# Optimization experiments

Hardware: AMD Instinct MI355X
Metric: run time of the kernel (lower is better)

The kernel has to match this reference:

```python
import jax, jax.numpy as jnp
import numpy as np

N_NODES = 50000
N_EDGES = 800000
IN_CH = 128
OUT_CH = 64
SELF_LOOP_W = 2.0  # improved=True in GCNConv


def setup_inputs() -> dict:
    key = jax.random.key(0)
    k1, k2, k3, k4 = jax.random.split(key, 4)
    x = jax.random.normal(k1, (N_NODES, IN_CH), dtype=jnp.float32)
    edge_index = jax.random.randint(k2, (2, N_EDGES), 0, N_NODES, dtype=jnp.int64)
    edge_weight = jax.random.uniform(k3, (N_EDGES,), dtype=jnp.float32)
    W = jax.random.normal(k4, (IN_CH, OUT_CH), dtype=jnp.float32) / np.sqrt(IN_CH)
    b = jnp.zeros((OUT_CH,), dtype=jnp.float32)
    return {"x": x, "edge_index": edge_index, "edge_weight": edge_weight, "W": W, "b": b}


def reference(x, edge_index, edge_weight, W, b):
    # Only the first GCNConv layer runs (the torch loop returns after k=0).
    N = x.shape[0]
    row, col = edge_index[0], edge_index[1]  # source, target

    # gcn_norm with add_self_loops=True, improved=True (fill value 2.0)
    loop_idx = jnp.arange(N, dtype=edge_index.dtype)
    row_f = jnp.concatenate([row, loop_idx])
    col_f = jnp.concatenate([col, loop_idx])
    ew_f = jnp.concatenate([edge_weight, jnp.full((N,), SELF_LOOP_W, dtype=edge_weight.dtype)])

    deg = jax.ops.segment_sum(ew_f, col_f, num_segments=N)          # [N]
    dinv = jnp.where(deg > 0, jax.lax.rsqrt(deg), 0.0)
    norm = dinv[row_f] * ew_f * dinv[col_f]                          # [E+N]

    # linear transform then normalized sparse aggregation
    xw = x @ W                                                       # [N, out]
    msg = norm[:, None] * xw[row_f]                                  # [E+N, out] gather
    out = jax.ops.segment_sum(msg, col_f, num_segments=N)           # [N, out] scatter-add
    return out + b
```

## Files before the change

kernel.cpp:

```cpp
#include <hip/hip_runtime.h>

constexpr int N    = 50000;
constexpr int E    = 800000;
constexpr int CIN  = 128;
constexpr int COUT = 64;
constexpr float SELF_LOOP_W = 2.0f;

constexpr int NB   = (N + 63) / 64;
constexpr int CAP  = 1536;
constexpr int EPB  = 2048;
constexpr int PBLK = (E + EPB - 1) / EPB;

typedef float          vfloat4  __attribute__((ext_vector_type(4)));
typedef int            vint2    __attribute__((ext_vector_type(2)));
typedef int            vint4    __attribute__((ext_vector_type(4)));
typedef unsigned short vushort4 __attribute__((ext_vector_type(4)));

__device__ __forceinline__ unsigned short f2bf(float f) {
    unsigned int u = __float_as_uint(f);
    u += 0x7FFFu + ((u >> 16) & 1u);
    return (unsigned short)(u >> 16);
}
__device__ __forceinline__ float bf2f(unsigned short h) {
    return __uint_as_float(((unsigned int)h) << 16);
}

__global__ __launch_bounds__(512) void partition_kernel(const int* __restrict__ row,
                                                        const int* __restrict__ col,
                                                        const float* __restrict__ ew,
                                                        int* __restrict__ bcur,
                                                        vint2* __restrict__ pk) {
    __shared__ int lhist[NB];
    __shared__ int lbase[NB];
    const int t  = threadIdx.x;
    const int e  = blockIdx.x * EPB + t * 4;
    const bool valid = (e < E);

    for (int i = t; i < NB; i += 512) lhist[i] = 0;
    __syncthreads();

    vint4 c4;
    if (valid) {
        c4 = *(const vint4*)(col + e);
        #pragma unroll
        for (int u = 0; u < 4; ++u) atomicAdd(&lhist[c4[u] >> 6], 1);
    }
    __syncthreads();

    for (int i = t; i < NB; i += 512) {
        int h = lhist[i];
        if (h > 0) lbase[i] = i * CAP + atomicAdd(&bcur[i], h);
    }
    __syncthreads();

    if (valid) {
        vint4   r4 = *(const vint4*)(row + e);
        vfloat4 w4 = *(const vfloat4*)(ew + e);
        #pragma unroll
        for (int u = 0; u < 4; ++u) {
            int c   = c4[u];
            int bkt = c >> 6;
            int p   = atomicAdd(&lbase[bkt], 1);
            if (p < (bkt + 1) * CAP) {
                vint2 v;
                v.x = r4[u] | ((c & 63) << 20);
                v.y = __float_as_int(w4[u]);
                pk[p] = v;
            }
        }
    }
}

__global__ __launch_bounds__(256) void xw_deg_kernel(const float* __restrict__ x,
                                                     const float* __restrict__ W,
                                                     const int* __restrict__ bcur,
                                                     const vint2* __restrict__ pk,
                                                     unsigned short* __restrict__ xwh,
                                                     float* __restrict__ dinv) {
    __shared__ __align__(16) float xs[64][132];
    __shared__ float ldeg[64];

    const int t    = threadIdx.x;
    const int b    = blockIdx.x;
    const int base = b * 64;

    #pragma unroll
    for (int i = 0; i < 8; ++i) {
        int f4  = i * 256 + t;
        int r   = f4 >> 5;
        int c4  = f4 & 31;
        int node = base + r;
        if (node >= N) node = N - 1;
        vfloat4 v = *(const vfloat4*)(x + (size_t)node * CIN + c4 * 4);
        *(vfloat4*)&xs[r][c4 * 4] = v;
    }
    if (t < 64) ldeg[t] = 0.f;
    __syncthreads();

    const int tc = t & 15;
    const int tn = t >> 4;

    float acc[4][4];
    #pragma unroll
    for (int i = 0; i < 4; ++i)
        #pragma unroll
        for (int j = 0; j < 4; ++j) acc[i][j] = 0.f;

    const float* Wp = W + tc * 4;
    #pragma unroll 8
    for (int k = 0; k < CIN; ++k) {
        vfloat4 bv = *(const vfloat4*)(Wp + (size_t)k * COUT);
        float a0 = xs[tn * 4 + 0][k];
        float a1 = xs[tn * 4 + 1][k];
        float a2 = xs[tn * 4 + 2][k];
        float a3 = xs[tn * 4 + 3][k];
        #pragma unroll
        for (int j = 0; j < 4; ++j) {
            acc[0][j] += a0 * bv[j];
            acc[1][j] += a1 * bv[j];
            acc[2][j] += a2 * bv[j];
            acc[3][j] += a3 * bv[j];
        }
    }

    #pragma unroll
    for (int i = 0; i < 4; ++i) {
        int node = base + tn * 4 + i;
        if (node >= N) continue;
        vushort4 hv;
        #pragma unroll
        for (int j = 0; j < 4; ++j) hv[j] = f2bf(acc[i][j]);
        *(vushort4*)(xwh + (size_t)node * COUT + tc * 4) = hv;
    }

    const int pbase = b * CAP;
    const int cnt   = min(bcur[b], CAP);
    for (int j = t; j < cnt; j += 256) {
        vint2 v = pk[pbase + j];
        atomicAdd(&ldeg[(v.x >> 20) & 63], __int_as_float(v.y));
    }
    __syncthreads();
    int node = base + t;
    if (t < 64 && node < N) dinv[node] = rsqrtf(SELF_LOOP_W + ldeg[t]);
}

__global__ __launch_bounds__(512) void aggregate_kernel(const int* __restrict__ bcur,
                                                        const vint2* __restrict__ pk,
                                                        const float* __restrict__ dinv,
                                                        const unsigned short* __restrict__ xwh,
                                                        const float* __restrict__ bias,
                                                        float* __restrict__ out) {
    __shared__ int   rawx[CAP];
    __shared__ float rawn[CAP];
    __shared__ int   s_r[CAP];
    __shared__ float s_n[CAP];
    __shared__ int   lhist[64], lofs[64], lcur[64];

    const int t    = threadIdx.x;
    const int lane = t & 63;
    const int wv   = t >> 6;
    const int b    = blockIdx.x;
    const int base = b * CAP;
    const int cnt  = min(bcur[b], CAP);

    if (t < 64) lhist[t] = 0;
    __syncthreads();

    for (int j = t; j < cnt; j += 512) {
        vint2 v = pk[base + j];
        rawx[j] = v.x;
        rawn[j] = __int_as_float(v.y) * dinv[v.x & 0xFFFFF];
        atomicAdd(&lhist[(v.x >> 20) & 63], 1);
    }
    __syncthreads();

    if (t < 64) {
        int v = lhist[t];
        int s = v;
        #pragma unroll
        for (int d = 1; d < 64; d <<= 1) {
            int u = __shfl_up(s, d);
            if (lane >= d) s += u;
        }
        lofs[t] = s - v;
        lcur[t] = s - v;
    }
    __syncthreads();

    for (int j = t; j < cnt; j += 512) {
        int xv = rawx[j];
        int p  = atomicAdd(&lcur[(xv >> 20) & 63], 1);
        s_r[p] = xv & 0xFFFFF;
        s_n[p] = rawn[j];
    }
    __syncthreads();

    const int q  = lane >> 4;
    const int c4 = lane & 15;

    for (int nd = wv; nd < 64; nd += 8) {
        int node = b * 64 + nd;
        if (node >= N) continue;
        int s0 = lofs[nd];
        int e0 = s0 + lhist[nd];

        float a0 = 0.f, a1 = 0.f, a2 = 0.f, a3 = 0.f;
        for (int i = s0; i < e0; i += 16) {
            int rr[4]; float nn[4]; vushort4 vv[4];
            #pragma unroll
            for (int u = 0; u < 4; ++u) {
                int j = i + 4 * u + q;
                bool ok = (j < e0);
                rr[u] = ok ? s_r[j] : s_r[s0];
                nn[u] = ok ? s_n[j] : 0.f;
            }
            #pragma unroll
            for (int u = 0; u < 4; ++u)
                vv[u] = *(const vushort4*)(xwh + (size_t)rr[u] * COUT + c4 * 4);
            #pragma unroll
            for (int u = 0; u < 4; ++u) {
                a0 += nn[u] * bf2f(vv[u][0]);
                a1 += nn[u] * bf2f(vv[u][1]);
                a2 += nn[u] * bf2f(vv[u][2]);
                a3 += nn[u] * bf2f(vv[u][3]);
            }
        }
        a0 += __shfl_xor(a0, 16); a0 += __shfl_xor(a0, 32);
        a1 += __shfl_xor(a1, 16); a1 += __shfl_xor(a1, 32);
        a2 += __shfl_xor(a2, 16); a2 += __shfl_xor(a2, 32);
        a3 += __shfl_xor(a3, 16); a3 += __shfl_xor(a3, 32);

        if (q == 0) {
            float dc = dinv[node];
            float s2 = SELF_LOOP_W * dc * dc;
            vushort4 sh = *(const vushort4*)(xwh + (size_t)node * COUT + c4 * 4);
            vfloat4  bv = *(const vfloat4*)(bias + c4 * 4);
            vfloat4  o;
            o[0] = dc * a0 + s2 * bf2f(sh[0]) + bv[0];
            o[1] = dc * a1 + s2 * bf2f(sh[1]) + bv[1];
            o[2] = dc * a2 + s2 * bf2f(sh[2]) + bv[2];
            o[3] = dc * a3 + s2 * bf2f(sh[3]) + bv[3];
            *(vfloat4*)(out + (size_t)node * COUT + c4 * 4) = o;
        }
    }
}

extern "C" void kernel_launch(void* const* d_in, const int* in_sizes, int n_in,
                              void* d_out, int out_size, void* d_ws, size_t ws_size,
                              hipStream_t stream) {
    const float* x  = (const float*)d_in[0];
    const int*   ei = (const int*)d_in[1];
    const float* ew = (const float*)d_in[2];
    const float* W  = (const float*)d_in[3];
    const float* b  = (const float*)d_in[4];
    float* out = (float*)d_out;

    unsigned short* xwh  = (unsigned short*)d_ws;
    float*          dinv = (float*)(xwh + (size_t)N * COUT);
    int*            bcur = (int*)(dinv + N);
    vint2*          pk   = (vint2*)(bcur + NB + 2);

    const int* rowp = ei;
    const int* colp = ei + E;

    hipMemsetAsync(bcur, 0, NB * sizeof(int), stream);
    partition_kernel<<<PBLK, 512, 0, stream>>>(rowp, colp, ew, bcur, pk);
    xw_deg_kernel   <<<NB, 256, 0, stream>>>(x, W, bcur, pk, xwh, dinv);
    aggregate_kernel<<<NB, 512, 0, stream>>>(bcur, pk, dinv, xwh, b, out);
}
```

Baseline: 149.9 us.

## Fuse edge partitioning with XW transform and compute degrees via global atomics

Merges the partition kernel and the xw/degree kernel into one launch with NB blocks, each handling 64 nodes of the XW product and 1024 edges of partitioning. Degree is now accumulated with global float atomics during partitioning, and rsqrt is computed on the fly in the aggregate kernel instead of storing dinv. This removes a launch and a second pass over the packed edge buffer, but adds 800K global atomics and repeated rsqrt/deg gathers in aggregation.

```diff
diff --git a/kernel.cpp b/kernel.cpp
--- a/kernel.cpp
+++ b/kernel.cpp
@@ -8,12 +8,10 @@
 
 constexpr int NB   = (N + 63) / 64;
 constexpr int CAP  = 1536;
-constexpr int EPB  = 2048;
-constexpr int PBLK = (E + EPB - 1) / EPB;
 
 typedef float          vfloat4  __attribute__((ext_vector_type(4)));
+typedef float          vfloat2  __attribute__((ext_vector_type(2)));
 typedef int            vint2    __attribute__((ext_vector_type(2)));
-typedef int            vint4    __attribute__((ext_vector_type(4)));
 typedef unsigned short vushort4 __attribute__((ext_vector_type(4)));
 
 __device__ __forceinline__ unsigned short f2bf(float f) {
@@ -25,25 +23,48 @@
     return __uint_as_float(((unsigned int)h) << 16);
 }
 
-__global__ __launch_bounds__(512) void partition_kernel(const int* __restrict__ row,
-                                                        const int* __restrict__ col,
-                                                        const float* __restrict__ ew,
-                                                        int* __restrict__ bcur,
-                                                        vint2* __restrict__ pk) {
+__global__ __launch_bounds__(512) void partition_xw_kernel(
+        const int* __restrict__ row, const int* __restrict__ col,
+        const float* __restrict__ ew, const float* __restrict__ x,
+        const float* __restrict__ W,
+        int* __restrict__ bcur, float* __restrict__ deg,
+        vint2* __restrict__ pk, unsigned short* __restrict__ xwh) {
     __shared__ int lhist[NB];
     __shared__ int lbase[NB];
-    const int t  = threadIdx.x;
-    const int e  = blockIdx.x * EPB + t * 4;
-    const bool valid = (e < E);
-
+    __shared__ __align__(16) float xs[64][132];
+
+    const int t    = threadIdx.x;
+    const int b    = blockIdx.x;
+    const int base = b * 64;
+
+    #pragma unroll
+    for (int i = 0; i < 4; ++i) {
+        int f4 = i * 512 + t;
+        int r  = f4 >> 5;
+        int c4 = f4 & 31;
+        int node = base + r;
+        if (node >= N) node = N - 1;
+        *(vfloat4*)&xs[r][c4 * 4] = *(const vfloat4*)(x + (size_t)node * CIN + c4 * 4);
+    }
     for (int i = t; i < NB; i += 512) lhist[i] = 0;
-    __syncthreads();
-
-    vint4 c4;
+
+    const int e0 = b * 1024 + t * 2;
+    const bool valid = (e0 < E);
+    vint2 c2 = {0, 0}, r2 = {0, 0};
+    vfloat2 w2 = {0.f, 0.f};
     if (valid) {
-        c4 = *(const vint4*)(col + e);
-        #pragma unroll
-        for (int u = 0; u < 4; ++u) atomicAdd(&lhist[c4[u] >> 6], 1);
+        c2 = *(const vint2*)(col + e0);
+        r2 = *(const vint2*)(row + e0);
+        w2 = *(const vfloat2*)(ew + e0);
+    }
+    __syncthreads();
+
+    if (valid) {
+        #pragma unroll
+        for (int u = 0; u < 2; ++u) {
+            atomicAdd(&lhist[c2[u] >> 6], 1);
+            atomicAdd(&deg[c2[u]], w2[u]);
+        }
     }
     __syncthreads();
 
@@ -54,55 +75,25 @@
     __syncthreads();
 
     if (valid) {
-        vint4   r4 = *(const vint4*)(row + e);
-        vfloat4 w4 = *(const vfloat4*)(ew + e);
-        #pragma unroll
-        for (int u = 0; u < 4; ++u) {
-            int c   = c4[u];
+        #pragma unroll
+        for (int u = 0; u < 2; ++u) {
+            int c   = c2[u];
             int bkt = c >> 6;
             int p   = atomicAdd(&lbase[bkt], 1);
             if (p < (bkt + 1) * CAP) {
                 vint2 v;
-                v.x = r4[u] | ((c & 63) << 20);
-                v.y = __float_as_int(w4[u]);
+                v.x = r2[u] | ((c & 63) << 20);
+                v.y = __float_as_int(w2[u]);
                 pk[p] = v;
             }
         }
     }
-}
-
-__global__ __launch_bounds__(256) void xw_deg_kernel(const float* __restrict__ x,
-                                                     const float* __restrict__ W,
-                                                     const int* __restrict__ bcur,
-                                                     const vint2* __restrict__ pk,
-                                                     unsigned short* __restrict__ xwh,
-                                                     float* __restrict__ dinv) {
-    __shared__ __align__(16) float xs[64][132];
-    __shared__ float ldeg[64];
-
-    const int t    = threadIdx.x;
-    const int b    = blockIdx.x;
-    const int base = b * 64;
-
-    #pragma unroll
-    for (int i = 0; i < 8; ++i) {
-        int f4  = i * 256 + t;
-        int r   = f4 >> 5;
-        int c4  = f4 & 31;
-        int node = base + r;
-        if (node >= N) node = N - 1;
-        vfloat4 v = *(const vfloat4*)(x + (size_t)node * CIN + c4 * 4);
-        *(vfloat4*)&xs[r][c4 * 4] = v;
-    }
-    if (t < 64) ldeg[t] = 0.f;
-    __syncthreads();
 
     const int tc = t & 15;
     const int tn = t >> 4;
-
-    float acc[4][4];
+    float acc[2][4];
     #pragma unroll
-    for (int i = 0; i < 4; ++i)
+    for (int i = 0; i < 2; ++i)
         #pragma unroll
         for (int j = 0; j < 4; ++j) acc[i][j] = 0.f;
 
@@ -110,43 +101,29 @@
     #pragma unroll 8
     for (int k = 0; k < CIN; ++k) {
         vfloat4 bv = *(const vfloat4*)(Wp + (size_t)k * COUT);
-        float a0 = xs[tn * 4 + 0][k];
-        float a1 = xs[tn * 4 + 1][k];
-        float a2 = xs[tn * 4 + 2][k];
-        float a3 = xs[tn * 4 + 3][k];
+        float a0 = xs[tn * 2 + 0][k];
+        float a1 = xs[tn * 2 + 1][k];
         #pragma unroll
         for (int j = 0; j < 4; ++j) {
             acc[0][j] += a0 * bv[j];
             acc[1][j] += a1 * bv[j];
-            acc[2][j] += a2 * bv[j];
-            acc[3][j] += a3 * bv[j];
         }
     }
 
     #pragma unroll
-    for (int i = 0; i < 4; ++i) {
-        int node = base + tn * 4 + i;
+    for (int i = 0; i < 2; ++i) {
+        int node = base + tn * 2 + i;
         if (node >= N) continue;
         vushort4 hv;
         #pragma unroll
         for (int j = 0; j < 4; ++j) hv[j] = f2bf(acc[i][j]);
         *(vushort4*)(xwh + (size_t)node * COUT + tc * 4) = hv;
     }
-
-    const int pbase = b * CAP;
-    const int cnt   = min(bcur[b], CAP);
-    for (int j = t; j < cnt; j += 256) {
-        vint2 v = pk[pbase + j];
-        atomicAdd(&ldeg[(v.x >> 20) & 63], __int_as_float(v.y));
-    }
-    __syncthreads();
-    int node = base + t;
-    if (t < 64 && node < N) dinv[node] = rsqrtf(SELF_LOOP_W + ldeg[t]);
 }
 
 __global__ __launch_bounds__(512) void aggregate_kernel(const int* __restrict__ bcur,
                                                         const vint2* __restrict__ pk,
-                                                        const float* __restrict__ dinv,
+                                                        const float* __restrict__ deg,
                                                         const unsigned short* __restrict__ xwh,
                                                         const float* __restrict__ bias,
                                                         float* __restrict__ out) {
@@ -169,7 +146,8 @@
     for (int j = t; j < cnt; j += 512) {
         vint2 v = pk[base + j];
         rawx[j] = v.x;
-        rawn[j] = __int_as_float(v.y) * dinv[v.x & 0xFFFFF];
+        float dg = deg[v.x & 0xFFFFF];
+        rawn[j] = __int_as_float(v.y) * rsqrtf(SELF_LOOP_W + dg);
         atomicAdd(&lhist[(v.x >> 20) & 63], 1);
     }
     __syncthreads();
@@ -231,7 +209,7 @@
         a3 += __shfl_xor(a3, 16); a3 += __shfl_xor(a3, 32);
 
         if (q == 0) {
-            float dc = dinv[node];
+            float dc = rsqrtf(SELF_LOOP_W + deg[node]);
             float s2 = SELF_LOOP_W * dc * dc;
             vushort4 sh = *(const vushort4*)(xwh + (size_t)node * COUT + c4 * 4);
             vfloat4  bv = *(const vfloat4*)(bias + c4 * 4);
@@ -256,15 +234,14 @@
     float* out = (float*)d_out;
 
     unsigned short* xwh  = (unsigned short*)d_ws;
-    float*          dinv = (float*)(xwh + (size_t)N * COUT);
-    int*            bcur = (int*)(dinv + N);
+    float*          deg  = (float*)(xwh + (size_t)N * COUT);
+    int*            bcur = (int*)(deg + N);
     vint2*          pk   = (vint2*)(bcur + NB + 2);
 
     const int* rowp = ei;
     const int* colp = ei + E;
 
-    hipMemsetAsync(bcur, 0, NB * sizeof(int), stream);
-    partition_kernel<<<PBLK, 512, 0, stream>>>(rowp, colp, ew, bcur, pk);
-    xw_deg_kernel   <<<NB, 256, 0, stream>>>(x, W, bcur, pk, xwh, dinv);
-    aggregate_kernel<<<NB, 512, 0, stream>>>(bcur, pk, dinv, xwh, b, out);
-}
+    hipMemsetAsync(deg, 0, (size_t)(N + NB + 2) * sizeof(int), stream);
+    partition_xw_kernel<<<NB, 512, 0, stream>>>(rowp, colp, ew, x, W, bcur, deg, pk, xwh);
+    aggregate_kernel   <<<NB, 512, 0, stream>>>(bcur, pk, deg, xwh, b, out);
+}
```

Result: slower. 195.0 us (+30.0%).
